# Kernel tuning notes

Hardware: AMD Instinct MI355X
Metric: run time of the kernel (lower is better)

## Reference

```python
import jax, jax.numpy as jnp
import numpy as np

N, K, D = 65536, 8192, 256

def setup_inputs() -> dict:
    key = jax.random.key(0)
    k1, k2 = jax.random.split(key)
    z = jax.random.normal(k1, (N, D), dtype=jnp.float32)
    # torch init: uniform(-1/K, 1/K)
    emb_w = jax.random.uniform(k2, (K, D), dtype=jnp.float32, minval=-1.0 / K, maxval=1.0 / K)
    return {"z": z, "emb_w": emb_w}

def reference(z, emb_w):
    # distance[n,k] = ||z_n||^2 + ||e_k||^2 - 2 z_n . e_k  (argmin is gradient-free)
    z2 = jnp.sum(z * z, axis=1, keepdims=True)            # [N,1]
    e2 = jnp.sum(emb_w * emb_w, axis=1)                    # [K]
    distance = z2 + e2 - 2.0 * (z @ emb_w.T)               # [N,K]
    indices = jnp.argmin(distance, axis=-1)                # [N]
    quantized = emb_w[indices]                             # [N,D]
    straight_through = jax.lax.stop_gradient(quantized - z) + z
    return quantized, straight_through, indices
```

## Files before the change

### kernel.cpp

```cpp
#include <hip/hip_runtime.h>
#include <hip/hip_fp16.h>

#define N_TOK 65536
#define K_EMB 8192
#define D_DIM 256
#define LIST_CAP 12288
#define CAND_CAP 16384

typedef unsigned short u16;
typedef unsigned int u32;
typedef unsigned long long u64;
typedef _Float16 f16x8 __attribute__((ext_vector_type(8)));
typedef float f32x16 __attribute__((ext_vector_type(16)));

__device__ __forceinline__ u16 f2h(float f) {
  union { _Float16 h; u16 u; } c; c.h = (_Float16)f; return c.u;
}
__device__ __forceinline__ f16x8 as_f16x8(uint4 v) {
  union { uint4 u; f16x8 h; } c; c.u = v; return c.h;
}
__device__ __forceinline__ void gld_lds16(const u16* g, u16* l) {
  __builtin_amdgcn_global_load_lds((const __attribute__((address_space(1))) void*)g,
                                   (__attribute__((address_space(3))) void*)l,
                                   16, 0, 0);
}

__global__ void vq_prep(const float* __restrict__ emb, u16* __restrict__ ehh,
                        float* __restrict__ e2f, u16* __restrict__ e2h,
                        int* __restrict__ count, int* __restrict__ candcount) {
  if (blockIdx.x == 0 && threadIdx.x == 0) { *count = 0; *candcount = 0; }
  const int w = threadIdx.x >> 6, lane = threadIdx.x & 63;
  const int k = blockIdx.x * 4 + w;
  const float4 v = ((const float4*)(emb + (size_t)k * D_DIM))[lane];
  uint2 p;
  p.x = (u32)f2h(v.x * 524288.0f) | ((u32)f2h(v.y * 524288.0f) << 16);
  p.y = (u32)f2h(v.z * 524288.0f) | ((u32)f2h(v.w * 524288.0f) << 16);
  ((uint2*)(ehh + (size_t)k * D_DIM))[lane] = p;
  double s = (double)v.x * v.x + (double)v.y * v.y +
             (double)v.z * v.z + (double)v.w * v.w;
  #pragma unroll
  for (int off = 32; off > 0; off >>= 1) s += __shfl_down(s, off);
  if (lane == 0) { e2f[k] = (float)s; e2h[k] = f2h(-(float)s * 16777216.0f); }
}

__launch_bounds__(512, 2)
__global__ void vq_phase1(const float* __restrict__ zg, const u16* __restrict__ ehh,
                          const u16* __restrict__ e2h, float* __restrict__ z2f,
                          int* __restrict__ idx1_ws, int* __restrict__ thrbuf,
                          u64* __restrict__ refbuf, int* __restrict__ list,
                          int* __restrict__ count) {
  __shared__ u16 lds[4][16384];
  __shared__ u16 e2l[8192];
  __shared__ float z2s[256];

  const int tid  = threadIdx.x;
  const int w    = tid >> 6;
  const int lane = tid & 63;
  const int q    = w & 1;
  const int g    = w >> 1;
  const int col  = lane & 31;
  const int h    = lane >> 5;
  const int n0   = blockIdx.x * 256 + g * 64;

  #pragma unroll
  for (int i = 0; i < 2; ++i) {
    int pp = w * 2 + i;
    gld_lds16(e2h + pp * 512 + lane * 8, &e2l[pp * 512]);
  }

  uint4 zres0[16], zres1[16];
  double zs0 = 0.0, zs1 = 0.0;
#define P1_ZLOAD(ZR, ZS, S) { \
    const float4* zp_ = (const float4*)(zg + (size_t)(n0 + (S) * 32 + col) * D_DIM); \
    _Pragma("unroll") \
    for (int c = 0; c < 16; ++c) { \
      float4 a_ = zp_[c * 4 + h * 2]; \
      float4 b_ = zp_[c * 4 + h * 2 + 1]; \
      ZS += (double)a_.x * a_.x + (double)a_.y * a_.y + \
            (double)a_.z * a_.z + (double)a_.w * a_.w; \
      ZS += (double)b_.x * b_.x + (double)b_.y * b_.y + \
            (double)b_.z * b_.z + (double)b_.w * b_.w; \
      uint4 u_; \
      u_.x = (u32)f2h(a_.x * 64.0f) | ((u32)f2h(a_.y * 64.0f) << 16); \
      u_.y = (u32)f2h(a_.z * 64.0f) | ((u32)f2h(a_.w * 64.0f) << 16); \
      u_.z = (u32)f2h(b_.x * 64.0f) | ((u32)f2h(b_.y * 64.0f) << 16); \
      u_.w = (u32)f2h(b_.z * 64.0f) | ((u32)f2h(b_.w * 64.0f) << 16); \
      ZR[c] = u_; \
    } }
  P1_ZLOAD(zres0, zs0, 0);
  P1_ZLOAD(zres1, zs1, 1);
#undef P1_ZLOAD
  zs0 += __shfl_xor(zs0, 32);
  zs1 += __shfl_xor(zs1, 32);
  if (lane < 32) {
    z2s[g * 64 + col]      = (float)zs0;  z2f[n0 + col]      = (float)zs0;
    z2s[g * 64 + 32 + col] = (float)zs1;  z2f[n0 + 32 + col] = (float)zs1;
  }

  uint4 bone = {0, 0, 0, 0};
  if (h == 0) bone.x = 0x3C00u;

  int m1[2] = {(int)0x80000000, (int)0x80000000};
  int m2[2] = {(int)0x80000000, (int)0x80000000};

#define P1_STAGE(T) { \
    _Pragma("unroll") \
    for (int i = 0; i < 4; ++i) { \
      int pp_ = w * 4 + i, qs_ = pp_ >> 4, cs_ = pp_ & 15; \
      gld_lds16(ehh + (size_t)((T) * 64 + qs_ * 32 + col) * D_DIM + cs_ * 16 + h * 8, \
                &lds[(T) & 3][qs_ * 8192 + cs_ * 512]); \
    } }
#define P1_STEP(T) { \
    const u16* lb_ = &lds[(T) & 3][q * 8192]; \
    uint4 ea_ = {0, 0, 0, 0}; \
    if (h == 0) ea_.x = (u32)e2l[(T) * 64 + q * 32 + col]; \
    f32x16 a0_ = {}, a1_ = {}; \
    __builtin_amdgcn_s_setprio(1); \
    _Pragma("unroll") \
    for (int c = 0; c < 16; ++c) { \
      f16x8 af_ = as_f16x8(*(const uint4*)(lb_ + c * 512 + lane * 8)); \
      a0_ = __builtin_amdgcn_mfma_f32_32x32x16_f16(af_, as_f16x8(zres0[c]), a0_, 0, 0, 0); \
      a1_ = __builtin_amdgcn_mfma_f32_32x32x16_f16(af_, as_f16x8(zres1[c]), a1_, 0, 0, 0); \
    } \
    a0_ = __builtin_amdgcn_mfma_f32_32x32x16_f16(as_f16x8(ea_), as_f16x8(bone), a0_, 0, 0, 0); \
    a1_ = __builtin_amdgcn_mfma_f32_32x32x16_f16(as_f16x8(ea_), as_f16x8(bone), a1_, 0, 0, 0); \
    __builtin_amdgcn_s_setprio(0); \
    const int bi_ = 4095 - (T) * 32 - q * 16; \
    _Pragma("unroll") \
    for (int r = 0; r < 16; ++r) { \
      int ka_ = ((int)a0_[r] << 12) + (bi_ - r); \
      m2[0] = max(m2[0], min(m1[0], ka_)); \
      m1[0] = max(m1[0], ka_); \
      int kb_ = ((int)a1_[r] << 12) + (bi_ - r); \
      m2[1] = max(m2[1], min(m1[1], kb_)); \
      m1[1] = max(m1[1], kb_); \
    } }

  P1_STAGE(0); P1_STAGE(1); P1_STAGE(2);
  for (int t = 0; t < 125; ++t) {
    asm volatile("s_waitcnt vmcnt(8)" ::: "memory");
    asm volatile("s_barrier" ::: "memory");
    P1_STAGE(t + 3);
    P1_STEP(t);
  }
  asm volatile("s_waitcnt vmcnt(8)" ::: "memory");
  asm volatile("s_barrier" ::: "memory");
  P1_STEP(125);
  asm volatile("s_waitcnt vmcnt(4)" ::: "memory");
  asm volatile("s_barrier" ::: "memory");
  P1_STEP(126);
  asm volatile("s_waitcnt vmcnt(0)" ::: "memory");
  asm volatile("s_barrier" ::: "memory");
  P1_STEP(127);
#undef P1_STAGE
#undef P1_STEP

  int k1d[2];
  #pragma unroll
  for (int s = 0; s < 2; ++s) {
    int x = 4095 - (m1[s] & 4095);
    int kt = x >> 5, kq = (x >> 4) & 1, kr = x & 15;
    k1d[s] = kt * 64 + kq * 32 + (kr & 3) + 8 * (kr >> 2) + 4 * h;
    int o1 = __shfl_xor(m1[s], 32), o2 = __shfl_xor(m2[s], 32);
    int ok1 = __shfl_xor(k1d[s], 32);
    bool take = (o1 > m1[s]) || (o1 == m1[s] && ok1 < k1d[s]);
    int loser = take ? m1[s] : o1;
    if (take) { m1[s] = o1; k1d[s] = ok1; }
    m2[s] = max(m2[s], max(o2, loser));
  }

  __syncthreads();
  int* rm1 = (int*)&lds[0][0];
  int* rk1 = (int*)&lds[0][1024];
  int* rm2 = (int*)&lds[0][2048];
  if (lane < 32) {
    #pragma unroll
    for (int s = 0; s < 2; ++s) {
      int nl = q * 256 + g * 64 + s * 32 + col;
      rm1[nl] = m1[s]; rk1[nl] = k1d[s]; rm2[nl] = m2[s];
    }
  }
  __syncthreads();
  if (tid < 256) {
    int a1 = rm1[tid], a2 = rm2[tid], ak = rk1[tid];
    int c1 = rm1[256 + tid], c2 = rm2[256 + tid], ck = rk1[256 + tid];
    bool take = (c1 > a1) || (c1 == a1 && ck < ak);
    int M1 = take ? c1 : a1;
    int K1 = take ? ck : ak;
    int M2 = max(max(a2, c2), take ? a1 : c1);
    int n = blockIdx.x * 256 + tid;
    int M1a = M1 >> 12, M2a = M2 >> 12;
    int e = (int)((__float_as_uint(z2s[tid] + 0.01f) >> 23) & 255);
    e = min(max(e, 127), 140);
    int bin = 1 << (e - 126);
    int p = 0;
    if ((M1a - M2a) < (bin * 2 + 128)) {
      int pos = atomicAdd(count, 1);
      if (pos < LIST_CAP) {
        list[pos] = n;
        thrbuf[pos] = M1a - (bin + 256);
        refbuf[pos] = 0xFFFFFFFFFFFFFFFFULL;
        p = pos + 1;
      }
    }
    idx1_ws[n] = K1 | (p << 13);
  }
}

__launch_bounds__(512, 2)
__global__ void vq_cand(const float* __restrict__ zg, const u16* __restrict__ ehh,
                        const u16* __restrict__ e2h, const int* __restrict__ count,
                        const int* __restrict__ list, const int* __restrict__ thrbuf,
                        u32* __restrict__ candbuf, int* __restrict__ candcount) {
  __shared__ u16 lds[2][32768];
  int cnt = *count; if (cnt > LIST_CAP) cnt = LIST_CAP;
  const int rt = blockIdx.x >> 2;
  const int ks = blockIdx.x & 3;
  if (rt * 64 >= cnt) return;
  const int k0 = ks * 2048;
  const int tid = threadIdx.x, w = tid >> 6, lane = tid & 63;
  const int q = w & 3, g = w >> 2;
  const int col = lane & 31, h = lane >> 5;
  const int ct = rt * 64 + g * 32 + col;
  const bool valid = ct < cnt;
  const int n_tok = valid ? (list[ct] & (N_TOK - 1)) : 0;
  const int thr = valid ? thrbuf[ct] : 0x7FFFFFFF;

  uint4 zres[16];
  {
    const float4* zp = (const float4*)(zg + (size_t)n_tok * D_DIM);
    #pragma unroll
    for (int c = 0; c < 16; ++c) {
      float4 a = zp[c * 4 + h * 2];
      float4 b2 = zp[c * 4 + h * 2 + 1];
      uint4 u;
      u.x = (u32)f2h(a.x * 64.0f) | ((u32)f2h(a.y * 64.0f) << 16);
      u.y = (u32)f2h(a.z * 64.0f) | ((u32)f2h(a.w * 64.0f) << 16);
      u.z = (u32)f2h(b2.x * 64.0f) | ((u32)f2h(b2.y * 64.0f) << 16);
      u.w = (u32)f2h(b2.z * 64.0f) | ((u32)f2h(b2.w * 64.0f) << 16);
      zres[c] = u;
    }
  }
  uint4 bone = {0, 0, 0, 0};
  if (h == 0) bone.x = 0x3C00u;

  #pragma unroll
  for (int i = 0; i < 8; ++i) {
    int p2 = w * 8 + i, qs = p2 >> 4, cs = p2 & 15;
    gld_lds16(ehh + (size_t)(k0 + qs * 32 + col) * D_DIM + cs * 16 + h * 8,
              &lds[0][qs * 8192 + cs * 512]);
  }

  for (int tK = 0; tK < 16; ++tK) {
    const int b = tK & 1;
    __syncthreads();
    if (tK + 1 < 16) {
      const int nb = b ^ 1, kb2 = k0 + (tK + 1) * 128;
      #pragma unroll
      for (int i = 0; i < 8; ++i) {
        int p2 = w * 8 + i, qs = p2 >> 4, cs = p2 & 15;
        gld_lds16(ehh + (size_t)(kb2 + qs * 32 + col) * D_DIM + cs * 16 + h * 8,
                  &lds[nb][qs * 8192 + cs * 512]);
      }
    }
    const int kb = k0 + tK * 128 + q * 32;
    uint4 ea = {0, 0, 0, 0};
    if (h == 0) ea.x = (u32)e2h[kb + col];
    const u16* lb = &lds[b][q * 8192];
    f32x16 acc = {};
    #pragma unroll
    for (int c = 0; c < 16; ++c) {
      f16x8 a = as_f16x8(*(const uint4*)(lb + c * 512 + lane * 8));
      acc = __builtin_amdgcn_mfma_f32_32x32x16_f16(a, as_f16x8(zres[c]), acc, 0, 0, 0);
    }
    acc = __builtin_amdgcn_mfma_f32_32x32x16_f16(as_f16x8(ea), as_f16x8(bone), acc, 0, 0, 0);
    #pragma unroll
    for (int r = 0; r < 16; ++r) {
      if ((int)acc[r] >= thr) {
        int kg = kb + (r & 3) + 8 * (r >> 2) + 4 * h;
        int pos = atomicAdd(candcount, 1);
        if (pos < CAND_CAP) candbuf[pos] = ((u32)ct << 13) | (u32)kg;
      }
    }
  }
}

__global__ void vq_refine2(const float* __restrict__ zg, const float* __restrict__ emb,
                           const float* __restrict__ z2f, const float* __restrict__ e2f,
                           const int* __restrict__ list, const int* __restrict__ candcount,
                           const u32* __restrict__ candbuf, u64* __restrict__ refbuf) {
  const int w = threadIdx.x >> 6, lane = threadIdx.x & 63;
  int ccnt = *candcount; if (ccnt > CAND_CAP) ccnt = CAND_CAP;
  for (int i = blockIdx.x * 4 + w; i < ccnt; i += gridDim.x * 4) {
    const u32 rec = candbuf[i];
    const int p = (int)(rec >> 13), k = (int)(rec & 8191u);
    const int n = list[p] & (N_TOK - 1);
    float4 zv = ((const float4*)(zg + (size_t)n * D_DIM))[lane];
    float4 ev = ((const float4*)(emb + (size_t)k * D_DIM))[lane];
    double s = (double)zv.x * ev.x + (double)zv.y * ev.y +
               (double)zv.z * ev.z + (double)zv.w * ev.w;
    #pragma unroll
    for (int off = 32; off > 0; off >>= 1) s += __shfl_down(s, off);
    if (lane == 0) {
      float S = z2f[n] + e2f[k];
      float val = S - 2.0f * (float)s;
      u64 key = ((u64)__float_as_uint(val) << 13) | (u64)k;
      atomicMin((unsigned long long*)(refbuf + p), (unsigned long long)key);
    }
  }
}

__global__ void vq_gather(const float* __restrict__ emb, const int* __restrict__ idx1_ws,
                          const u64* __restrict__ refbuf, float* __restrict__ out) {
  const int w = threadIdx.x >> 6, lane = threadIdx.x & 63;
  const int n = blockIdx.x * 4 + w;
  const int enc = idx1_ws[n];
  int idx = enc & 8191;
  const int p = enc >> 13;
  if (p > 0) {
    u64 rb = refbuf[p - 1];
    if (rb != 0xFFFFFFFFFFFFFFFFULL) idx = (int)(rb & 8191ULL);
  }
  float4 v = ((const float4*)(emb + (size_t)idx * D_DIM))[lane];
  float4* o = (float4*)out;
  o[(size_t)n * 64 + lane] = v;
  o[(size_t)4194304 + (size_t)n * 64 + lane] = v;
  if (lane == 0) out[(size_t)33554432 + n] = (float)idx;
}

extern "C" void kernel_launch(void* const* d_in, const int* in_sizes, int n_in,
                              void* d_out, int out_size, void* d_ws, size_t ws_size,
                              hipStream_t stream) {
  const float* z   = (const float*)d_in[0];
  const float* emb = (const float*)d_in[1];
  char* ws = (char*)d_ws;
  u16*   ehh       = (u16*)(ws);
  float* e2f       = (float*)(ws + 4194304);
  u16*   e2h       = (u16*)(ws + 4227072);
  float* z2f       = (float*)(ws + 4243456);
  int*   idx1_ws   = (int*)(ws + 4505600);
  u64*   refbuf    = (u64*)(ws + 4767744);
  int*   list      = (int*)(ws + 4866048);
  int*   thrbuf    = (int*)(ws + 4915200);
  u32*   candbuf   = (u32*)(ws + 4964352);
  int*   count     = (int*)(ws + 5029888);
  int*   candcount = (int*)(ws + 5029892);

  vq_prep   <<<K_EMB / 4, 256, 0, stream>>>(emb, ehh, e2f, e2h, count, candcount);
  vq_phase1 <<<N_TOK / 256, 512, 0, stream>>>(z, ehh, e2h, z2f, idx1_ws, thrbuf,
                                              refbuf, list, count);
  vq_cand   <<<768, 512, 0, stream>>>(z, ehh, e2h, count, list, thrbuf,
                                      candbuf, candcount);
  vq_refine2<<<512, 256, 0, stream>>>(z, emb, z2f, e2f, list, candcount,
                                      candbuf, refbuf);
  vq_gather <<<N_TOK / 4, 256, 0, stream>>>(emb, idx1_ws, refbuf, (float*)d_out);
}
```

Measured before the change: 689.3 us.

## Double-buffer MFMA accumulators to overlap argmin scan with next tile's matmul

Splits each phase-1 step into a compute part and a scan part, using two sets of accumulators so the top-2 scan of tile t-1 runs while the MFMAs of tile t are in flight. This hides the scalar compare chain behind matrix-core work. The extra accumulators raise register pressure, so launch bounds drop from 2 to 1 block per CU, which lowers occupancy. The setprio hints are also removed.

Result: slower. 766.1 us (+11.2%).

```diff
diff --git a/kernel.cpp b/kernel.cpp
--- a/kernel.cpp
+++ b/kernel.cpp
@@ -43,7 +43,7 @@
   if (lane == 0) { e2f[k] = (float)s; e2h[k] = f2h(-(float)s * 16777216.0f); }
 }
 
-__launch_bounds__(512, 2)
+__launch_bounds__(512, 1)
 __global__ void vq_phase1(const float* __restrict__ zg, const u16* __restrict__ ehh,
                           const u16* __restrict__ e2h, float* __restrict__ z2f,
                           int* __restrict__ idx1_ws, int* __restrict__ thrbuf,
@@ -102,6 +102,7 @@
 
   int m1[2] = {(int)0x80000000, (int)0x80000000};
   int m2[2] = {(int)0x80000000, (int)0x80000000};
+  f32x16 accA0 = {}, accA1 = {}, accB0 = {}, accB1 = {};
 
 #define P1_STAGE(T) { \
     _Pragma("unroll") \
@@ -110,50 +111,61 @@
       gld_lds16(ehh + (size_t)((T) * 64 + qs_ * 32 + col) * D_DIM + cs_ * 16 + h * 8, \
                 &lds[(T) & 3][qs_ * 8192 + cs_ * 512]); \
     } }
-#define P1_STEP(T) { \
+#define P1_COMPUTE(ACC0, ACC1, T) { \
     const u16* lb_ = &lds[(T) & 3][q * 8192]; \
     uint4 ea_ = {0, 0, 0, 0}; \
     if (h == 0) ea_.x = (u32)e2l[(T) * 64 + q * 32 + col]; \
-    f32x16 a0_ = {}, a1_ = {}; \
-    __builtin_amdgcn_s_setprio(1); \
     _Pragma("unroll") \
     for (int c = 0; c < 16; ++c) { \
       f16x8 af_ = as_f16x8(*(const uint4*)(lb_ + c * 512 + lane * 8)); \
-      a0_ = __builtin_amdgcn_mfma_f32_32x32x16_f16(af_, as_f16x8(zres0[c]), a0_, 0, 0, 0); \
-      a1_ = __builtin_amdgcn_mfma_f32_32x32x16_f16(af_, as_f16x8(zres1[c]), a1_, 0, 0, 0); \
+      ACC0 = __builtin_amdgcn_mfma_f32_32x32x16_f16(af_, as_f16x8(zres0[c]), ACC0, 0, 0, 0); \
+      ACC1 = __builtin_amdgcn_mfma_f32_32x32x16_f16(af_, as_f16x8(zres1[c]), ACC1, 0, 0, 0); \
     } \
-    a0_ = __builtin_amdgcn_mfma_f32_32x32x16_f16(as_f16x8(ea_), as_f16x8(bone), a0_, 0, 0, 0); \
-    a1_ = __builtin_amdgcn_mfma_f32_32x32x16_f16(as_f16x8(ea_), as_f16x8(bone), a1_, 0, 0, 0); \
-    __builtin_amdgcn_s_setprio(0); \
+    ACC0 = __builtin_amdgcn_mfma_f32_32x32x16_f16(as_f16x8(ea_), as_f16x8(bone), ACC0, 0, 0, 0); \
+    ACC1 = __builtin_amdgcn_mfma_f32_32x32x16_f16(as_f16x8(ea_), as_f16x8(bone), ACC1, 0, 0, 0); }
+#define P1_SCAN(ACC0, ACC1, T) { \
     const int bi_ = 4095 - (T) * 32 - q * 16; \
     _Pragma("unroll") \
     for (int r = 0; r < 16; ++r) { \
-      int ka_ = ((int)a0_[r] << 12) + (bi_ - r); \
+      int ka_ = ((int)ACC0[r] << 12) + (bi_ - r); \
       m2[0] = max(m2[0], min(m1[0], ka_)); \
       m1[0] = max(m1[0], ka_); \
-      int kb_ = ((int)a1_[r] << 12) + (bi_ - r); \
+      int kb_ = ((int)ACC1[r] << 12) + (bi_ - r); \
       m2[1] = max(m2[1], min(m1[1], kb_)); \
       m1[1] = max(m1[1], kb_); \
     } }
+#define P1_ZERO(ACC0, ACC1) { \
+    _Pragma("unroll") \
+    for (int r = 0; r < 16; ++r) { ACC0[r] = 0.0f; ACC1[r] = 0.0f; } }
+#define P1_WAIT(N) \
+    asm volatile("s_waitcnt vmcnt(" #N ")" ::: "memory"); \
+    asm volatile("s_barrier" ::: "memory");
 
   P1_STAGE(0); P1_STAGE(1); P1_STAGE(2);
-  for (int t = 0; t < 125; ++t) {
-    asm volatile("s_waitcnt vmcnt(8)" ::: "memory");
-    asm volatile("s_barrier" ::: "memory");
-    P1_STAGE(t + 3);
-    P1_STEP(t);
-  }
-  asm volatile("s_waitcnt vmcnt(8)" ::: "memory");
-  asm volatile("s_barrier" ::: "memory");
-  P1_STEP(125);
-  asm volatile("s_waitcnt vmcnt(4)" ::: "memory");
-  asm volatile("s_barrier" ::: "memory");
-  P1_STEP(126);
-  asm volatile("s_waitcnt vmcnt(0)" ::: "memory");
-  asm volatile("s_barrier" ::: "memory");
-  P1_STEP(127);
+  P1_WAIT(8); P1_STAGE(3);
+  P1_COMPUTE(accA0, accA1, 0);
+  for (int t = 1; t < 125; t += 2) {
+    P1_WAIT(8); P1_STAGE(t + 3);
+    P1_COMPUTE(accB0, accB1, t);
+    P1_SCAN(accA0, accA1, t - 1);
+    P1_ZERO(accA0, accA1);
+    P1_WAIT(8); P1_STAGE(t + 4);
+    P1_COMPUTE(accA0, accA1, t + 1);
+    P1_SCAN(accB0, accB1, t);
+    P1_ZERO(accB0, accB1);
+  }
+  P1_WAIT(8);
+  P1_COMPUTE(accB0, accB1, 125); P1_SCAN(accA0, accA1, 124); P1_ZERO(accA0, accA1);
+  P1_WAIT(4);
+  P1_COMPUTE(accA0, accA1, 126); P1_SCAN(accB0, accB1, 125); P1_ZERO(accB0, accB1);
+  P1_WAIT(0);
+  P1_COMPUTE(accB0, accB1, 127); P1_SCAN(accA0, accA1, 126);
+  P1_SCAN(accB0, accB1, 127);
 #undef P1_STAGE
-#undef P1_STEP
+#undef P1_COMPUTE
+#undef P1_SCAN
+#undef P1_ZERO
+#undef P1_WAIT
 
   int k1d[2];
   #pragma unroll
```
